# Optimization experiments

Measured on AMD Instinct MI355X. Metric: run time of the kernel, lower is better.

Reference implementation:

```python
import jax, jax.numpy as jnp
import numpy as np
from jax import lax

D, DIM, FF, V, B, S = 8, 1024, 4096, 32000, 2, 2048
EPS = 1e-6

def _rms(x, w):
    return x * lax.rsqrt(jnp.mean(x * x, axis=-1, keepdims=True) + EPS) * w

def _lin(x, W, b):
    # torch nn.Linear: weight [out, in]
    return x @ W.T + b

def _comb(e1, e2):
    # associative op for h_t = a_t * h_{t-1} + b_t  (h_0 = 0)
    a1, b1 = e1
    a2, b2 = e2
    return a1 * a2, a2 * b1 + b2

def _forward(tokens, emb, h0, Wf, bf, Wi, bi, Wig, big, Wog, bog, n1, n2, Wfc, bfc, Wfa, bfa, Wfo, bfo, nl, Wout, bout):
    # embedding with max_norm=1 renorm semantics
    e = emb[tokens]                                  # [B,S,DIM]
    nrm = jnp.linalg.norm(e, axis=-1, keepdims=True)
    x = jnp.where(nrm > 1.0, e / (nrm + 1e-7), e)
    for i in range(D):
        # --- QuasiLSTM sub-block ---
        x_ = x
        h_in = _rms(x, n1[i])
        f = jax.nn.sigmoid(_lin(h_in, Wf[i], bf[i]))                 # forget gate [B,S,DIM]
        v = jnp.tanh(_lin(h_in, Wi[i], bi[i])) * jax.nn.sigmoid(_lin(h_in, Wig[i], big[i]))
        _, h_inner = lax.associative_scan(_comb, (f, v), axis=1)     # inner-chunk scan (zero init)
        h = h_inner + h0[i][None, None, :] * jnp.cumprod(f, axis=1)  # cross-chunk from last_hidden_init
        y = jnp.tanh(h) * jax.nn.sigmoid(_lin(h_in, Wog[i], bog[i]))
        x = y + x_                                                   # dropout(p) is identity in eval
        # --- SwiGLU FFN sub-block ---
        x_ = x
        z = _rms(x, n2[i])
        u = _lin(z, Wfc[i], bfc[i]) * jax.nn.silu(_lin(z, Wfa[i], bfa[i]))
        x = _lin(u, Wfo[i], bfo[i]) + x_
    x = _rms(x, nl)
    return _lin(x, Wout, bout)                                       # [B,S,V]

def setup_inputs() -> dict:
    key = jax.random.key(0)
    ks = jax.random.split(key, 16)
    n = lambda k, s: jax.random.normal(k, s, jnp.float32) * 0.02
    zD = jnp.zeros((D, DIM), jnp.float32)
    return {
        "tokens": jax.random.randint(ks[0], (B, S), 0, V),
        "emb": n(ks[1], (V, DIM)),
        "h0": jax.random.normal(ks[2], (D, DIM), jnp.float32),
        "Wf": n(ks[3], (D, DIM, DIM)), "bf": zD,
        "Wi": n(ks[4], (D, DIM, DIM)), "bi": zD,
        "Wig": n(ks[5], (D, DIM, DIM)), "big": zD,
        "Wog": n(ks[6], (D, DIM, DIM)), "bog": zD,
        "n1": jnp.ones((D, DIM), jnp.float32),
        "n2": jnp.ones((D, DIM), jnp.float32),
        "Wfc": n(ks[7], (D, FF, DIM)), "bfc": jnp.zeros((D, FF), jnp.float32),
        "Wfa": n(ks[8], (D, FF, DIM)), "bfa": jnp.zeros((D, FF), jnp.float32),
        "Wfo": n(ks[9], (D, DIM, FF)), "bfo": zD,
        "nl": jnp.ones((DIM,), jnp.float32),
        "Wout": n(ks[10], (V, DIM)), "bout": jnp.zeros((V,), jnp.float32),
    }

def reference(tokens, emb, h0, Wf, bf, Wi, bi, Wig, big, Wog, bog, n1, n2, Wfc, bfc, Wfa, bfa, Wfo, bfo, nl, Wout, bout):
    return _forward(tokens, emb, h0, Wf, bf, Wi, bi, Wig, big, Wog, bog, n1, n2, Wfc, bfc, Wfa, bfa, Wfo, bfo, nl, Wout, bout)
```

## Files before the change

### kernel.cpp

```cpp
#include <hip/hip_runtime.h>
#include <hip/hip_bf16.h>
#include <cstdint>
#include <cstddef>

typedef unsigned short u16;
typedef __attribute__((ext_vector_type(4))) float f32x4;
typedef __attribute__((ext_vector_type(8))) short bf16x8;
typedef __attribute__((ext_vector_type(8))) unsigned short u16x8;
typedef __attribute__((ext_vector_type(4))) unsigned short u16x4;

#define D_LAYERS 8
#define DIMN 1024
#define FFD 4096
#define VOCAB 32000
#define MROWS 4096
#define SEQ 2048
#define NCHUNK 64
#define LCHUNK 32

__device__ __forceinline__ u16 f2b(float f) {
  union { float f; unsigned u; } v; v.f = f;
  unsigned r = v.u + 0x7FFFu + ((v.u >> 16) & 1u);
  return (u16)(r >> 16);
}
__device__ __forceinline__ float b2f(u16 h) {
  union { unsigned u; float f; } v; v.u = ((unsigned)h) << 16;
  return v.f;
}
__device__ __forceinline__ float sigm(float x) { return 1.f / (1.f + __expf(-x)); }
__device__ __forceinline__ float ftanh(float x) {
  float e = __expf(2.f * x);
  return 1.f - 2.f / (e + 1.f);
}

__device__ __forceinline__ void async16(const void* g, void* l) {
  auto gp = reinterpret_cast<const __attribute__((address_space(1))) char*>(
      reinterpret_cast<uintptr_t>(g));
  auto lp = reinterpret_cast<__attribute__((address_space(3))) char*>(
      reinterpret_cast<uintptr_t>(l));
  __builtin_amdgcn_global_load_lds(gp, lp, 16, 0, 0);
}

__device__ __forceinline__ float blk_sum(float v) {
  __shared__ float sm[4];
  #pragma unroll
  for (int o = 32; o > 0; o >>= 1) v += __shfl_xor(v, o);
  if ((threadIdx.x & 63) == 0) sm[threadIdx.x >> 6] = v;
  __syncthreads();
  float r = sm[0] + sm[1] + sm[2] + sm[3];
  __syncthreads();
  return r;
}

__global__ __launch_bounds__(256) void k_cvt(const f32x4* __restrict__ in,
                                             u16x8* __restrict__ out) {
  size_t i = (size_t)blockIdx.x * 256 + threadIdx.x;
  f32x4 a = in[i * 2], b = in[i * 2 + 1];
  u16x8 o;
  o[0] = f2b(a[0]); o[1] = f2b(a[1]); o[2] = f2b(a[2]); o[3] = f2b(a[3]);
  o[4] = f2b(b[0]); o[5] = f2b(b[1]); o[6] = f2b(b[2]); o[7] = f2b(b[3]);
  out[i] = o;
}

__global__ __launch_bounds__(256) void k_cvt7(
    const float* __restrict__ Wf, const float* __restrict__ Wi,
    const float* __restrict__ Wig, const float* __restrict__ Wog,
    const float* __restrict__ Wfc, const float* __restrict__ Wfa,
    const float* __restrict__ Wfo,
    u16* __restrict__ dGates,
    u16* __restrict__ dFc, u16* __restrict__ dFa, u16* __restrict__ dFo,
    int L)
{
  const int b = blockIdx.x;
  const float* src; u16* dst; size_t off;
  if (b < 2048) {
    const int g = b >> 9, r = b & 511;
    const float* s = (g == 0) ? Wf : (g == 1) ? Wi : (g == 2) ? Wig : Wog;
    src = s + (size_t)L * 1048576;
    dst = dGates + (size_t)g * 1048576;
    off = (size_t)r * 2048;
  } else if (b < 4096) {
    src = Wfc + (size_t)L * 4194304; dst = dFc; off = (size_t)(b - 2048) * 2048;
  } else if (b < 6144) {
    src = Wfa + (size_t)L * 4194304; dst = dFa; off = (size_t)(b - 4096) * 2048;
  } else {
    src = Wfo + (size_t)L * 4194304; dst = dFo; off = (size_t)(b - 6144) * 2048;
  }
  const size_t i = off + (size_t)threadIdx.x * 8;
  f32x4 a = *(const f32x4*)(src + i);
  f32x4 c = *(const f32x4*)(src + i + 4);
  u16x8 o;
  o[0] = f2b(a[0]); o[1] = f2b(a[1]); o[2] = f2b(a[2]); o[3] = f2b(a[3]);
  o[4] = f2b(c[0]); o[5] = f2b(c[1]); o[6] = f2b(c[2]); o[7] = f2b(c[3]);
  *(u16x8*)(dst + i) = o;
}

__global__ __launch_bounds__(256) void k_embed(const int* __restrict__ tok,
                                               const float* __restrict__ emb,
                                               float* __restrict__ x) {
  const int r = blockIdx.x;
  const int tk = tok[r];
  f32x4 v = ((const f32x4*)(emb + (size_t)tk * DIMN))[threadIdx.x];
  float ss = v[0]*v[0] + v[1]*v[1] + v[2]*v[2] + v[3]*v[3];
  float tot = blk_sum(ss);
  float nrm = sqrtf(tot);
  float s = (nrm > 1.f) ? (1.f / (nrm + 1e-7f)) : 1.f;
  f32x4 o = {v[0]*s, v[1]*s, v[2]*s, v[3]*s};
  ((f32x4*)(x + (size_t)r * DIMN))[threadIdx.x] = o;
}

__global__ __launch_bounds__(256) void k_rms(const float* __restrict__ x,
                                             const float* __restrict__ wgt,
                                             u16* __restrict__ out) {
  const int r = blockIdx.x;
  f32x4 v = ((const f32x4*)(x + (size_t)r * DIMN))[threadIdx.x];
  float ss = v[0]*v[0] + v[1]*v[1] + v[2]*v[2] + v[3]*v[3];
  float tot = blk_sum(ss);
  float sc = rsqrtf(tot * (1.f / DIMN) + 1e-6f);
  f32x4 w = ((const f32x4*)wgt)[threadIdx.x];
  u16x4 o;
  o[0] = f2b(v[0] * sc * w[0]);
  o[1] = f2b(v[1] * sc * w[1]);
  o[2] = f2b(v[2] * sc * w[2]);
  o[3] = f2b(v[3] * sc * w[3]);
  ((u16x4*)(out + (size_t)r * DIMN))[threadIdx.x] = o;
}

__global__ __launch_bounds__(256) void k_scanA(const float* __restrict__ f,
                                               const float* __restrict__ v,
                                               float* __restrict__ Ac,
                                               float* __restrict__ Vc) {
  const int bx = blockIdx.x;
  const int dg = bx & 3, c = (bx >> 2) & 63, b = bx >> 8;
  const int d = dg * 256 + threadIdx.x;
  const size_t base = ((size_t)(b * SEQ + c * LCHUNK)) * DIMN + d;
  float a = 1.f, h = 0.f;
  #pragma unroll 4
  for (int t = 0; t < LCHUNK; ++t) {
    size_t ix = base + (size_t)t * DIMN;
    float fv = f[ix];
    h = fv * h + v[ix];
    a *= fv;
  }
  const size_t ci = ((size_t)(b * NCHUNK + c)) * DIMN + d;
  Ac[ci] = a; Vc[ci] = h;
}

__global__ __launch_bounds__(256) void k_scanBC(const float* __restrict__ f,
                                                const float* __restrict__ v,
                                                const float* __restrict__ oo,
                                                const float* __restrict__ Ac,
                                                const float* __restrict__ Vc,
                                                const float* __restrict__ h0,
                                                float* __restrict__ x) {
  const int bx = blockIdx.x;
  const int dg = bx & 3, c = (bx >> 2) & 63, b = bx >> 8;
  const int d = dg * 256 + threadIdx.x;
  float h = h0[d];
  for (int cc = 0; cc < c; ++cc) {
    const size_t ci = ((size_t)(b * NCHUNK + cc)) * DIMN + d;
    h = Ac[ci] * h + Vc[ci];
  }
  const size_t base = ((size_t)(b * SEQ + c * LCHUNK)) * DIMN + d;
  for (int t = 0; t < LCHUNK; ++t) {
    size_t ix = base + (size_t)t * DIMN;
    float fv = f[ix];
    h = fv * h + v[ix];
    x[ix] += ftanh(h) * oo[ix];
  }
}

__global__ __launch_bounds__(256) void k_redrms(const f32x4* __restrict__ pp,
                                                const float* __restrict__ bias,
                                                const float* __restrict__ wgt,
                                                float* __restrict__ x,
                                                u16* __restrict__ hin) {
  const int r = blockIdx.x;
  const size_t i = (size_t)r * 256 + threadIdx.x;
  const int n4 = threadIdx.x;
  f32x4 a = pp[i];
  f32x4 b = pp[i + (size_t)MROWS * DIMN / 4];
  f32x4 bs = ((const f32x4*)bias)[n4];
  f32x4 xv = ((const f32x4*)x)[i];
  f32x4 o = {xv[0] + a[0] + b[0] + bs[0], xv[1] + a[1] + b[1] + bs[1],
             xv[2] + a[2] + b[2] + bs[2], xv[3] + a[3] + b[3] + bs[3]};
  ((f32x4*)x)[i] = o;
  float ss = o[0]*o[0] + o[1]*o[1] + o[2]*o[2] + o[3]*o[3];
  float tot = blk_sum(ss);
  float sc = rsqrtf(tot * (1.f / DIMN) + 1e-6f);
  f32x4 w = ((const f32x4*)wgt)[n4];
  u16x4 hh;
  hh[0] = f2b(o[0] * sc * w[0]);
  hh[1] = f2b(o[1] * sc * w[1]);
  hh[2] = f2b(o[2] * sc * w[2]);
  hh[3] = f2b(o[3] * sc * w[3]);
  ((u16x4*)(hin + (size_t)r * DIMN))[n4] = hh;
}

constexpr int EPI_BIAS_F32 = 4, EPI_PART = 5;

template<int BN_T, int EPI>
__global__ __launch_bounds__(256, 2)
void gemm_bt(const u16* __restrict__ A,
             const u16* __restrict__ B0,
             const float* __restrict__ bias0,
             float* __restrict__ oF0,
             int N, int K, int LD)
{
  constexpr int MF = (BN_T == 128) ? 4 : 2;
  constexpr int WAVES_N = (BN_T == 128) ? 2 : 1;
  constexpr int ISS_B = BN_T / 32;
  __shared__ __align__(16) u16 As[128 * 64];
  __shared__ __align__(16) u16 Bs[BN_T * 64];
  const int tid = threadIdx.x;
  const int w = tid >> 6, lane = tid & 63;
  const int wm = w / WAVES_N, wn = w % WAVES_N;
  const int m0 = blockIdx.x * 128;
  const int n0 = blockIdx.y * BN_T;

  const u16* Aw = A;
  const u16* Bw = B0;
  float* oF = oF0;
  if constexpr (EPI == EPI_PART) {
    const int koff = blockIdx.z * K;
    Aw += koff; Bw += koff;
    oF += (size_t)blockIdx.z * MROWS * DIMN;
  }

  const f32x4 zero = {0.f, 0.f, 0.f, 0.f};
  f32x4 acc[MF][4];
  #pragma unroll
  for (int mf = 0; mf < MF; ++mf)
    #pragma unroll
    for (int nf = 0; nf < 4; ++nf) acc[mf][nf] = zero;

  for (int kt = 0; kt < K; kt += 64) {
    #pragma unroll
    for (int i = 0; i < 4; ++i) {
      int p = i * 4096 + w * 1024 + lane * 16;
      int r = p >> 7;
      int cs = (p & 127) ^ ((r & 7) << 4);
      async16(Aw + ((size_t)(m0 + r) * LD + kt) + (cs >> 1),
              (char*)As + i * 4096 + w * 1024);
    }
    #pragma unroll
    for (int i = 0; i < ISS_B; ++i) {
      int p = i * 4096 + w * 1024 + lane * 16;
      int r = p >> 7;
      int cs = (p & 127) ^ ((r & 7) << 4);
      async16(Bw + ((size_t)(n0 + r) * LD + kt) + (cs >> 1),
              (char*)Bs + i * 4096 + w * 1024);
    }
    __syncthreads();
    #pragma unroll
    for (int ks = 0; ks < 2; ++ks) {
      bf16x8 av[MF], bv[4];
      const int cbase = ks * 64 + ((lane >> 4) << 4);
      #pragma unroll
      for (int mf = 0; mf < MF; ++mf) {
        int r = wm * (MF * 16) + mf * 16 + (lane & 15);
        av[mf] = *(const bf16x8*)((const char*)As + r * 128 + (cbase ^ ((r & 7) << 4)));
      }
      #pragma unroll
      for (int nf = 0; nf < 4; ++nf) {
        int r = wn * 64 + nf * 16 + (lane & 15);
        bv[nf] = *(const bf16x8*)((const char*)Bs + r * 128 + (cbase ^ ((r & 7) << 4)));
      }
      #pragma unroll
      for (int mf = 0; mf < MF; ++mf)
        #pragma unroll
        for (int nf = 0; nf < 4; ++nf)
          acc[mf][nf] = __builtin_amdgcn_mfma_f32_16x16x32_bf16(
              av[mf], bv[nf], acc[mf][nf], 0, 0, 0);
    }
    __syncthreads();
  }

  #pragma unroll
  for (int nf = 0; nf < 4; ++nf) {
    const int n = n0 + wn * 64 + nf * 16 + (lane & 15);
    const float bb = (EPI == EPI_PART) ? 0.f : bias0[n];
    #pragma unroll
    for (int mf = 0; mf < MF; ++mf) {
      #pragma unroll
      for (int j = 0; j < 4; ++j) {
        const int m = m0 + wm * (MF * 16) + mf * 16 + ((lane >> 4) << 2) + j;
        const size_t idx = (size_t)m * N + n;
        oF[idx] = acc[mf][nf][j] + bb;
      }
    }
  }
}

constexpr int EDG = 0, EDF = 1;

template<int EPI>
__global__ __launch_bounds__(256, 2)
void gemm_dual(const u16* __restrict__ A,
               const u16* __restrict__ Ba0, const u16* __restrict__ Bb0,
               const u16* __restrict__ Ba1, const u16* __restrict__ Bb1,
               const float* __restrict__ ba0, const float* __restrict__ bb0,
               const float* __restrict__ ba1, const float* __restrict__ bb1,
               float* __restrict__ oV,
               float* __restrict__ oFa, float* __restrict__ oFb,
               u16* __restrict__ oU,
               int N, int K)
{
  __shared__ __align__(16) u16 As[128 * 64];
  __shared__ __align__(16) u16 Bsa[128 * 64];
  __shared__ __align__(16) u16 Bsb[128 * 64];
  const int tid = threadIdx.x;
  const int w = tid >> 6, lane = tid & 63;
  const int wm = w >> 1, wn = w & 1;
  const int m0 = blockIdx.x * 128;
  const int n0 = blockIdx.y * 128;
  const int z = blockIdx.z;

  const u16* Ba = (EPI == EDG && z) ? Ba1 : Ba0;
  const u16* Bb = (EPI == EDG && z) ? Bb1 : Bb0;
  const float* ba = (EPI == EDG && z) ? ba1 : ba0;
  const float* bb = (EPI == EDG && z) ? bb1 : bb0;

  const f32x4 zero = {0.f, 0.f, 0.f, 0.f};
  f32x4 accA[4][4], accB[4][4];
  #pragma unroll
  for (int mf = 0; mf < 4; ++mf)
    #pragma unroll
    for (int nf = 0; nf < 4; ++nf) { accA[mf][nf] = zero; accB[mf][nf] = zero; }

  for (int kt = 0; kt < K; kt += 64) {
    #pragma unroll
    for (int i = 0; i < 4; ++i) {
      const int p = i * 4096 + w * 1024 + lane * 16;
      const int r = p >> 7;
      const int cs = (p & 127) ^ ((r & 7) << 4);
      async16(A  + ((size_t)(m0 + r) * K + kt) + (cs >> 1),
              (char*)As + i * 4096 + w * 1024);
      async16(Ba + ((size_t)(n0 + r) * K + kt) + (cs >> 1),
              (char*)Bsa + i * 4096 + w * 1024);
      async16(Bb + ((size_t)(n0 + r) * K + kt) + (cs >> 1),
              (char*)Bsb + i * 4096 + w * 1024);
    }
    __syncthreads();
    #pragma unroll
    for (int ks = 0; ks < 2; ++ks) {
      bf16x8 av[4], bva[4], bvb[4];
      const int cbase = ks * 64 + ((lane >> 4) << 4);
      #pragma unroll
      for (int mf = 0; mf < 4; ++mf) {
        const int r = wm * 64 + mf * 16 + (lane & 15);
        av[mf] = *(const bf16x8*)((const char*)As + r * 128 + (cbase ^ ((r & 7) << 4)));
      }
      #pragma unroll
      for (int nf = 0; nf < 4; ++nf) {
        const int r = wn * 64 + nf * 16 + (lane & 15);
        const int off = r * 128 + (cbase ^ ((r & 7) << 4));
        bva[nf] = *(const bf16x8*)((const char*)Bsa + off);
        bvb[nf] = *(const bf16x8*)((const char*)Bsb + off);
      }
      #pragma unroll
      for (int mf = 0; mf < 4; ++mf)
        #pragma unroll
        for (int nf = 0; nf < 4; ++nf) {
          accA[mf][nf] = __builtin_amdgcn_mfma_f32_16x16x32_bf16(
              av[mf], bva[nf], accA[mf][nf], 0, 0, 0);
          accB[mf][nf] = __builtin_amdgcn_mfma_f32_16x16x32_bf16(
              av[mf], bvb[nf], accB[mf][nf], 0, 0, 0);
        }
    }
    __syncthreads();
  }

  #pragma unroll
  for (int nf = 0; nf < 4; ++nf) {
    const int n = n0 + wn * 64 + nf * 16 + (lane & 15);
    const float bba = ba[n], bbb = bb[n];
    #pragma unroll
    for (int mf = 0; mf < 4; ++mf) {
      #pragma unroll
      for (int j = 0; j < 4; ++j) {
        const int m = m0 + wm * 64 + mf * 16 + ((lane >> 4) << 2) + j;
        const size_t idx = (size_t)m * N + n;
        const float va = accA[mf][nf][j] + bba;
        const float vb = accB[mf][nf][j] + bbb;
        if constexpr (EPI == EDG) {
          if (z == 0) {
            oV[idx] = ftanh(va) * sigm(vb);
          } else {
            oFa[idx] = sigm(va);
            oFb[idx] = sigm(vb);
          }
        } else {
          oU[idx] = f2b(vb * va * sigm(va));
        }
      }
    }
  }
}

extern "C" void kernel_launch(void* const* d_in, const int* in_sizes, int n_in,
                              void* d_out, int out_size, void* d_ws, size_t ws_size,
                              hipStream_t stream) {
  (void)in_sizes; (void)n_in; (void)out_size; (void)ws_size;
  const int*   tokens = (const int*)d_in[0];
  const float* emb  = (const float*)d_in[1];
  const float* h0   = (const float*)d_in[2];
  const float* Wf   = (const float*)d_in[3];
  const float* bf_  = (const float*)d_in[4];
  const float* Wi   = (const float*)d_in[5];
  const float* bi_  = (const float*)d_in[6];
  const float* Wig  = (const float*)d_in[7];
  const float* big_ = (const float*)d_in[8];
  const float* Wog  = (const float*)d_in[9];
  const float* bog_ = (const float*)d_in[10];
  const float* n1   = (const float*)d_in[11];
  const float* n2   = (const float*)d_in[12];
  const float* Wfc  = (const float*)d_in[13];
  const float* bfc_ = (const float*)d_in[14];
  const float* Wfa  = (const float*)d_in[15];
  const float* bfa_ = (const float*)d_in[16];
  const float* Wfo  = (const float*)d_in[17];
  const float* bfo_ = (const float*)d_in[18];
  const float* nl_  = (const float*)d_in[19];
  const float* Wout = (const float*)d_in[20];
  const float* bout_= (const float*)d_in[21];
  float* out = (float*)d_out;

  char* p = (char*)d_ws;
  auto alloc = [&](size_t bytes) {
    char* r = p; p += (bytes + 255) & ~(size_t)255; return r;
  };
  u16* wbGates = (u16*)alloc((size_t)4 * DIMN * DIMN * 2);
  u16* wbWfc  = (u16*)alloc((size_t)FFD * DIMN * 2);
  u16* wbWfa  = (u16*)alloc((size_t)FFD * DIMN * 2);
  u16* wbWfo  = (u16*)alloc((size_t)FFD * DIMN * 2);
  u16* wbWout = (u16*)alloc((size_t)VOCAB * DIMN * 2);
  float* x    = (float*)alloc((size_t)MROWS * DIMN * 4);
  u16* hin    = (u16*)alloc((size_t)MROWS * DIMN * 2);
  float* fbuf = (float*)alloc((size_t)MROWS * DIMN * 4);
  float* vbuf = (float*)alloc((size_t)MROWS * DIMN * 4);
  float* oobuf= (float*)alloc((size_t)MROWS * DIMN * 4);
  u16* ub     = (u16*)alloc((size_t)MROWS * FFD * 2);
  float* pk   = (float*)alloc((size_t)2 * MROWS * DIMN * 4);
  float* Ac    = (float*)alloc((size_t)2 * NCHUNK * DIMN * 4);
  float* Vc    = (float*)alloc((size_t)2 * NCHUNK * DIMN * 4);

  u16* wbWf  = wbGates;
  u16* wbWi  = wbGates + (size_t)1 * DIMN * DIMN;
  u16* wbWig = wbGates + (size_t)2 * DIMN * DIMN;
  u16* wbWog = wbGates + (size_t)3 * DIMN * DIMN;

  k_embed<<<dim3(MROWS), dim3(256), 0, stream>>>(tokens, emb, x);

  for (int L = 0; L < D_LAYERS; ++L) {
    k_cvt7<<<dim3(8192), dim3(256), 0, stream>>>(
        Wf, Wi, Wig, Wog, Wfc, Wfa, Wfo,
        wbGates, wbWfc, wbWfa, wbWfo, L);

    if (L == 0)
      k_rms<<<dim3(MROWS), dim3(256), 0, stream>>>(x, n1, hin);

    gemm_dual<EDG><<<dim3(32, 8, 2), dim3(256), 0, stream>>>(
        hin, wbWi, wbWig, wbWf, wbWog,
        bi_ + (size_t)L * DIMN, big_ + (size_t)L * DIMN,
        bf_ + (size_t)L * DIMN, bog_ + (size_t)L * DIMN,
        vbuf, fbuf, oobuf, nullptr, DIMN, DIMN);

    k_scanA<<<dim3(512), dim3(256), 0, stream>>>(fbuf, vbuf, Ac, Vc);
    k_scanBC<<<dim3(512), dim3(256), 0, stream>>>(
        fbuf, vbuf, oobuf, Ac, Vc, h0 + (size_t)L * DIMN, x);

    k_rms<<<dim3(MROWS), dim3(256), 0, stream>>>(x, n2 + (size_t)L * DIMN, hin);

    gemm_dual<EDF><<<dim3(32, 32, 1), dim3(256), 0, stream>>>(
        hin, wbWfa, wbWfc, nullptr, nullptr,
        bfa_ + (size_t)L * FFD, bfc_ + (size_t)L * FFD, nullptr, nullptr,
        nullptr, nullptr, nullptr, ub, FFD, DIMN);

    gemm_bt<128, EPI_PART><<<dim3(32, 8, 2), dim3(256), 0, stream>>>(
        ub, wbWfo, nullptr, pk, DIMN, FFD / 2, FFD);

    const float* wnext = (L + 1 < D_LAYERS) ? (n1 + (size_t)(L + 1) * DIMN) : nl_;
    k_redrms<<<dim3(MROWS), dim3(256), 0, stream>>>(
        (const f32x4*)pk, bfo_ + (size_t)L * DIMN, wnext, x, hin);
  }

  k_cvt<<<dim3(16000), dim3(256), 0, stream>>>((const f32x4*)Wout, (u16x8*)wbWout);
  gemm_bt<128, EPI_BIAS_F32><<<dim3(32, 250), dim3(256), 0, stream>>>(
      hin, wbWout, bout_, out, VOCAB, DIMN, DIMN);
}
```

Before: 2.102 ms.

## Store output gate as bf16 and run vocab projection through dual-B GEMM

The output-gate sigmoid is now written as bf16 instead of fp32, which halves that buffer's write and read traffic in the gate GEMM and the scan kernel. The final vocabulary projection moves from the single-B GEMM to the dual-B GEMM. Each block computes two 128-column tiles that are 16000 columns apart and shares one loaded A tile between them, so the grid is halved and A reuse increases. The trade-offs are slightly lower precision for the output gate and higher register and LDS pressure in the dual kernel.

```diff
diff --git a/kernel.cpp b/kernel.cpp
--- a/kernel.cpp
+++ b/kernel.cpp
@@ -148,7 +148,7 @@
 
 __global__ __launch_bounds__(256) void k_scanBC(const float* __restrict__ f,
                                                 const float* __restrict__ v,
-                                                const float* __restrict__ oo,
+                                                const u16* __restrict__ oo,
                                                 const float* __restrict__ Ac,
                                                 const float* __restrict__ Vc,
                                                 const float* __restrict__ h0,
@@ -166,7 +166,7 @@
     size_t ix = base + (size_t)t * DIMN;
     float fv = f[ix];
     h = fv * h + v[ix];
-    x[ix] += ftanh(h) * oo[ix];
+    x[ix] += ftanh(h) * b2f(oo[ix]);
   }
 }
 
@@ -197,7 +197,7 @@
   ((u16x4*)(hin + (size_t)r * DIMN))[n4] = hh;
 }
 
-constexpr int EPI_BIAS_F32 = 4, EPI_PART = 5;
+constexpr int EPI_PART = 5;
 
 template<int BN_T, int EPI>
 __global__ __launch_bounds__(256, 2)
@@ -279,20 +279,19 @@
   #pragma unroll
   for (int nf = 0; nf < 4; ++nf) {
     const int n = n0 + wn * 64 + nf * 16 + (lane & 15);
-    const float bb = (EPI == EPI_PART) ? 0.f : bias0[n];
     #pragma unroll
     for (int mf = 0; mf < MF; ++mf) {
       #pragma unroll
       for (int j = 0; j < 4; ++j) {
         const int m = m0 + wm * (MF * 16) + mf * 16 + ((lane >> 4) << 2) + j;
         const size_t idx = (size_t)m * N + n;
-        oF[idx] = acc[mf][nf][j] + bb;
-      }
-    }
-  }
-}
-
-constexpr int EDG = 0, EDF = 1;
+        oF[idx] = acc[mf][nf][j];
+      }
+    }
+  }
+}
+
+constexpr int EDG = 0, EDF = 1, EDV = 2;
 
 template<int EPI>
 __global__ __launch_bounds__(256, 2)
@@ -302,7 +301,7 @@
                const float* __restrict__ ba0, const float* __restrict__ bb0,
                const float* __restrict__ ba1, const float* __restrict__ bb1,
                float* __restrict__ oV,
-               float* __restrict__ oFa, float* __restrict__ oFb,
+               float* __restrict__ oFa,
                u16* __restrict__ oU,
                int N, int K)
 {
@@ -380,18 +379,23 @@
       #pragma unroll
       for (int j = 0; j < 4; ++j) {
         const int m = m0 + wm * 64 + mf * 16 + ((lane >> 4) << 2) + j;
-        const size_t idx = (size_t)m * N + n;
         const float va = accA[mf][nf][j] + bba;
         const float vb = accB[mf][nf][j] + bbb;
         if constexpr (EPI == EDG) {
+          const size_t idx = (size_t)m * N + n;
           if (z == 0) {
             oV[idx] = ftanh(va) * sigm(vb);
           } else {
             oFa[idx] = sigm(va);
-            oFb[idx] = sigm(vb);
+            oU[idx] = f2b(sigm(vb));
           }
+        } else if constexpr (EPI == EDF) {
+          const size_t idx = (size_t)m * N + n;
+          oU[idx] = f2b(vb * va * sigm(va));
         } else {
-          oU[idx] = f2b(vb * va * sigm(va));
+          const size_t idx = (size_t)m * VOCAB + n;
+          oFa[idx] = va;
+          oFa[idx + 16000] = vb;
         }
       }
     }
@@ -439,7 +443,7 @@
   u16* hin    = (u16*)alloc((size_t)MROWS * DIMN * 2);
   float* fbuf = (float*)alloc((size_t)MROWS * DIMN * 4);
   float* vbuf = (float*)alloc((size_t)MROWS * DIMN * 4);
-  float* oobuf= (float*)alloc((size_t)MROWS * DIMN * 4);
+  u16* oobuf  = (u16*)alloc((size_t)MROWS * DIMN * 2);
   u16* ub     = (u16*)alloc((size_t)MROWS * FFD * 2);
   float* pk   = (float*)alloc((size_t)2 * MROWS * DIMN * 4);
   float* Ac    = (float*)alloc((size_t)2 * NCHUNK * DIMN * 4);
@@ -464,7 +468,7 @@
         hin, wbWi, wbWig, wbWf, wbWog,
         bi_ + (size_t)L * DIMN, big_ + (size_t)L * DIMN,
         bf_ + (size_t)L * DIMN, bog_ + (size_t)L * DIMN,
-        vbuf, fbuf, oobuf, nullptr, DIMN, DIMN);
+        vbuf, fbuf, oobuf, DIMN, DIMN);
 
     k_scanA<<<dim3(512), dim3(256), 0, stream>>>(fbuf, vbuf, Ac, Vc);
     k_scanBC<<<dim3(512), dim3(256), 0, stream>>>(
@@ -475,7 +479,7 @@
     gemm_dual<EDF><<<dim3(32, 32, 1), dim3(256), 0, stream>>>(
         hin, wbWfa, wbWfc, nullptr, nullptr,
         bfa_ + (size_t)L * FFD, bfc_ + (size_t)L * FFD, nullptr, nullptr,
-        nullptr, nullptr, nullptr, ub, FFD, DIMN);
+        nullptr, nullptr, ub, FFD, DIMN);
 
     gemm_bt<128, EPI_PART><<<dim3(32, 8, 2), dim3(256), 0, stream>>>(
         ub, wbWfo, nullptr, pk, DIMN, FFD / 2, FFD);
@@ -486,6 +490,8 @@
   }
 
   k_cvt<<<dim3(16000), dim3(256), 0, stream>>>((const f32x4*)Wout, (u16x8*)wbWout);
-  gemm_bt<128, EPI_BIAS_F32><<<dim3(32, 250), dim3(256), 0, stream>>>(
-      hin, wbWout, bout_, out, VOCAB, DIMN, DIMN);
-}
+  gemm_dual<EDV><<<dim3(32, 125, 1), dim3(256), 0, stream>>>(
+      hin, wbWout, wbWout + (size_t)16000 * DIMN, nullptr, nullptr,
+      bout_, bout_ + 16000, nullptr, nullptr,
+      nullptr, out, nullptr, VOCAB, DIMN);
+}
```

After: 2.163 ms. 1.03x slower.
